# Kernel optimization log

Hardware: AMD Instinct MI355X
Metric: run time of the kernel (lower is better)

## Reference

```python
import jax, jax.numpy as jnp
import numpy as np

N = 100000   # nodes
F = 128      # feature dim (== numEdges ctor arg)
H = 64       # hidden_dim
E = 1600000  # edges (avg degree 16)


def setup_inputs() -> dict:
    key = jax.random.key(0)
    ks = jax.random.split(key, 8)
    x = jax.random.normal(ks[0], (N, F), dtype=jnp.float32)
    edge_index = jax.random.randint(ks[1], (2, E), 0, N)
    sF = 1.0 / np.sqrt(F)
    sH = 1.0 / np.sqrt(H)
    conv_W = jax.random.normal(ks[2], (F, F), dtype=jnp.float32) * sF  # GCNConv linear weight
    conv_b = jnp.zeros((F,), dtype=jnp.float32)
    w1 = jax.random.normal(ks[3], (H, F), dtype=jnp.float32) * sF
    b1 = jnp.zeros((H,), dtype=jnp.float32)
    w2 = jax.random.normal(ks[4], (H, H), dtype=jnp.float32) * sH
    b2 = jnp.zeros((H,), dtype=jnp.float32)
    w3 = jax.random.normal(ks[5], (1, H), dtype=jnp.float32) * sH
    b3 = jnp.zeros((1,), dtype=jnp.float32)
    return dict(x=x, edge_index=edge_index, conv_W=conv_W, conv_b=conv_b,
                w1=w1, b1=b1, w2=w2, b2=b2, w3=w3, b3=b3)


def reference(x, edge_index, conv_W, conv_b, w1, b1, w2, b2, w3, b3):
    n = x.shape[0]
    # --- GCNConv: D^{-1/2}(A+I)D^{-1/2} X W + b ---
    xw = x @ conv_W.T                                   # [N, F]
    loops = jnp.arange(n)
    src = jnp.concatenate([edge_index[0], loops])       # add self-loops
    dst = jnp.concatenate([edge_index[1], loops])
    deg = jax.ops.segment_sum(jnp.ones(src.shape[0], xw.dtype), dst, num_segments=n)
    dinv = jnp.where(deg > 0, jax.lax.rsqrt(deg), 0.0)
    norm = dinv[src] * dinv[dst]                        # [E+N]
    h = jax.ops.segment_sum(xw[src] * norm[:, None], dst, num_segments=n) + conv_b  # [N, F]
    # --- MedianAggregation (index=None -> single segment, 'lower' interpolation) ---
    med = jnp.sort(h, axis=0)[(n - 1) // 2][None, :]    # [1, F]
    # --- tanh MLP ---
    a = jnp.tanh(med @ w1.T + b1)
    a = jnp.tanh(a @ w2.T + b2)
    return a @ w3.T + b3                                # [1, 1]
```

## Files before the change

### kernel.cpp

```cpp
#include <hip/hip_runtime.h>
#include <math.h>


#define CAP    24576
#define NREG   8
#define RCAP   3072
#define MPT    24
#define CCAP   96
#define CSTR   97
#define DSTR   32
#define OVCAP  4096
#define SPCAP  2048
#define BCAP   4608
#define NBKMAX 400
#define CH     4096

typedef __attribute__((ext_vector_type(8))) short short8;
typedef __attribute__((ext_vector_type(4))) float f32x4;
typedef __attribute__((ext_vector_type(8))) _Float16 half8;
typedef __attribute__((ext_vector_type(2))) _Float16 half2v;

__device__ __forceinline__ unsigned ordKey(float x) {
    unsigned u = __float_as_uint(x);
    return (u & 0x80000000u) ? ~u : (u | 0x80000000u);
}
__device__ __forceinline__ unsigned short f2bf(float f) {
    unsigned u = __float_as_uint(f);
    return (unsigned short)((u + 0x7FFFu + ((u >> 16) & 1u)) >> 16);
}

__global__ void k_init(int* __restrict__ cursor, int* __restrict__ below8,
                       int* __restrict__ candCnt8, int* __restrict__ ovCnt,
                       const float* __restrict__ W, short* __restrict__ Whi,
                       short* __restrict__ Wlo, int nbk) {
    if (blockIdx.x == 1) {
        for (int idx = threadIdx.x; idx < 16384; idx += 256) {
            int j = idx & 7, lane = (idx >> 3) & 63;
            int t = (idx >> 9) & 7, s = idx >> 12;
            int row = t * 16 + (lane & 15);
            int k = s * 32 + (lane >> 4) * 8 + j;
            float w = W[row * 128 + k];
            unsigned short hb = f2bf(w);
            float hf = __uint_as_float((unsigned)hb << 16);
            Whi[idx] = (short)hb;
            Wlo[idx] = (short)f2bf(w - hf);
        }
        return;
    }
    int t = threadIdx.x;
    for (int i = t; i < nbk; i += 256) cursor[i] = 0;
    for (int i = t; i < NREG * 128; i += 256) { below8[i] = 0; candCnt8[i] = 0; }
    if (t == 0) { ovCnt[0] = 0; ovCnt[1] = 0; ovCnt[2] = 0; }
}

__global__ __launch_bounds__(256) void k_binGemm(
        const float* __restrict__ x, const short* __restrict__ Whi,
        const short* __restrict__ Wlo, _Float16* __restrict__ xw, int n, int GB,
        const int* __restrict__ src, const int* __restrict__ dst, int E,
        int* __restrict__ cursor, int2* __restrict__ binned,
        int* __restrict__ ovCnt, int2* __restrict__ ovBuf, int nbk) {
    __shared__ char smem[40960];
    const int t = threadIdx.x;
    if ((int)blockIdx.x < GB) {
        float* trn = (float*)smem;
        const int lane = t & 63, wv = t >> 6;
        const int quad = lane >> 4, m = lane & 15;
        const int rowBase = blockIdx.x * 64 + wv * 16;
        const int r = rowBase + m;
        const int rl = r < n ? r : (n - 1);
        f32x4 acc[8];
        #pragma unroll
        for (int q = 0; q < 8; q++) acc[q] = (f32x4){0.f, 0.f, 0.f, 0.f};
        #pragma unroll
        for (int s = 0; s < 4; s++) {
            const float* xp = x + (size_t)rl * 128 + s * 32 + quad * 8;
            float4 p0 = *(const float4*)xp;
            float4 p1 = *(const float4*)(xp + 4);
            float f[8] = {p0.x, p0.y, p0.z, p0.w, p1.x, p1.y, p1.z, p1.w};
            short8 ah, al;
            #pragma unroll
            for (int j = 0; j < 8; j++) {
                unsigned short hb = f2bf(f[j]);
                float hf = __uint_as_float((unsigned)hb << 16);
                ah[j] = (short)hb;
                al[j] = (short)f2bf(f[j] - hf);
            }
            #pragma unroll
            for (int q = 0; q < 8; q++) {
                short8 bh = *(const short8*)(Whi + (((s * 8 + q) * 64 + lane) << 3));
                short8 bl = *(const short8*)(Wlo + (((s * 8 + q) * 64 + lane) << 3));
                acc[q] = __builtin_amdgcn_mfma_f32_16x16x32_bf16(ah, bh, acc[q], 0, 0, 0);
                acc[q] = __builtin_amdgcn_mfma_f32_16x16x32_bf16(al, bh, acc[q], 0, 0, 0);
                acc[q] = __builtin_amdgcn_mfma_f32_16x16x32_bf16(ah, bl, acc[q], 0, 0, 0);
            }
        }
        float* tw = trn + wv * (16 * 132);
        #pragma unroll
        for (int q = 0; q < 8; q++)
            #pragma unroll
            for (int e = 0; e < 4; e++)
                tw[(quad * 4 + e) * 132 + q * 16 + m] = acc[q][e];
        #pragma unroll
        for (int i = 0; i < 4; i++) {
            int row = i * 4 + (lane >> 4);
            int c8 = lane & 15;
            const float* tp = tw + row * 132 + c8 * 8;
            float4 p0 = *(const float4*)tp;
            float4 p1 = *(const float4*)(tp + 4);
            half8 o;
            o[0] = (_Float16)p0.x; o[1] = (_Float16)p0.y;
            o[2] = (_Float16)p0.z; o[3] = (_Float16)p0.w;
            o[4] = (_Float16)p1.x; o[5] = (_Float16)p1.y;
            o[6] = (_Float16)p1.z; o[7] = (_Float16)p1.w;
            int grow = rowBase + row;
            if (grow < n) *(half8*)(xw + (size_t)grow * 128 + c8 * 8) = o;
        }
    } else {
        int2* sorted = (int2*)smem;
        int* hist  = (int*)(smem + 32768);
        int* gbase = hist + NBKMAX;
        int* lpre  = gbase + NBKMAX;
        int* hist2 = lpre + NBKMAX;
        int* sbase = hist2 + NBKMAX;
        int* wscan = sbase + NBKMAX;
        const int e0 = ((int)blockIdx.x - GB) * CH;
        const int len = min(CH, E - e0);
        for (int i = t; i < nbk; i += 256) { hist[i] = 0; hist2[i] = 0; }
        __syncthreads();
        for (int k = t; k < len; k += 256)
            atomicAdd(&hist[dst[e0 + k] >> 8], 1);
        __syncthreads();
        for (int i = t; i < nbk; i += 256) {
            int c = hist[i];
            if (c) {
                int g = atomicAdd(&cursor[i], c);
                if (g + c <= BCAP) gbase[i] = g;
                else {
                    gbase[i] = -1;
                    sbase[i] = atomicAdd(ovCnt, c);
                }
            }
        }
        {
            const int i0 = t * 2, i1 = i0 + 1;
            int h0 = (i0 < nbk) ? hist[i0] : 0;
            int h1 = (i1 < nbk) ? hist[i1] : 0;
            int s = h0 + h1;
            const int lane = t & 63, wv = t >> 6;
            int sc = s;
            #pragma unroll
            for (int off = 1; off < 64; off <<= 1) {
                int y = __shfl_up(sc, off, 64);
                if (lane >= off) sc += y;
            }
            if (lane == 63) wscan[wv] = sc;
            __syncthreads();
            int wbase = 0;
            for (int ww = 0; ww < wv; ww++) wbase += wscan[ww];
            int excl = wbase + sc - s;
            if (i0 < nbk) lpre[i0] = excl;
            if (i1 < nbk) lpre[i1] = excl + h0;
        }
        __syncthreads();
        for (int k = t; k < len; k += 256) {
            int s = src[e0 + k], d = dst[e0 + k];
            int b = d >> 8;
            int p = atomicAdd(&hist2[b], 1);
            sorted[lpre[b] + p] = make_int2(s, d);
        }
        __syncthreads();
        for (int k = t; k < len; k += 256) {
            int2 e = sorted[k];
            int b = e.y >> 8;
            int li = k - lpre[b];
            int g = gbase[b];
            if (g >= 0) binned[(size_t)b * BCAP + g + li] = e;
            else {
                int o = sbase[b] + li;
                if (o < OVCAP) ovBuf[o] = make_int2(e.y, e.x);
            }
        }
    }
}

__global__ __launch_bounds__(1024) void k_build(int2* __restrict__ binned,
                                                const int* __restrict__ cursor,
                                                float* __restrict__ dinv,
                                                unsigned char* __restrict__ deg8,
                                                int* __restrict__ ovCnt,
                                                int2* __restrict__ ovBuf,
                                                int* __restrict__ spillNodes, int n) {
    __shared__ int ladj[256 * DSTR];
    __shared__ int lcnt[256];
    const int b = blockIdx.x, t = threadIdx.x;
    const int cnt = min(cursor[b], BCAP);
    const size_t e0 = (size_t)b * BCAP;
    if (t < 256) lcnt[t] = 0;
    __syncthreads();
    for (int k = t; k < cnt; k += 1024) {
        int2 e = binned[e0 + k];
        int li = e.y & 255;
        int pos = atomicAdd(&lcnt[li], 1);
        if (pos < DSTR) ladj[li * DSTR + pos] = e.x;
        else {
            int o = atomicAdd(ovCnt, 1);
            if (o < OVCAP) ovBuf[o] = make_int2(e.y, e.x);
        }
    }
    __syncthreads();
    int4* adjOut = (int4*)((int*)binned + e0 * 2);
    const int4* lsrc4 = (const int4*)ladj;
    for (int i = t; i < 2048; i += 1024) adjOut[i] = lsrc4[i];
    if (t < 256) {
        int node = b * 256 + t;
        if (node < n) {
            int deg = lcnt[t];
            dinv[node] = (float)(1.0 / sqrt((double)(deg + 1)));
            deg8[node] = (unsigned char)(deg < 255 ? deg : 255);
            if (deg > DSTR) {
                int p = atomicAdd(ovCnt + 1, 1);
                if (p < SPCAP) spillNodes[p] = node;
            }
        }
    }
}

__global__ __launch_bounds__(256) void k_aggH(const _Float16* __restrict__ xw,
                                              const unsigned char* __restrict__ deg8,
                                              const int* __restrict__ adjAll,
                                              const float* __restrict__ dinv,
                                              const float* __restrict__ conv_b,
                                              _Float16* __restrict__ h, int n) {
    const int d = blockIdx.x * 4 + (threadIdx.x >> 6);
    if (d >= n) return;
    const int lane = threadIdx.x & 63;
    const int l32 = lane & 31;
    int degT = deg8[d];
    const int degB = degT < DSTR ? degT : DSTR;
    const float dd = dinv[d];
    const int* adjRow = adjAll + (size_t)(d >> 8) * (BCAP * 2) + (d & 255) * DSTR;
    int aj = adjRow[l32];
    bool ev = (lane < 32) && (l32 < degB);
    int ajs = ev ? aj : 0;
    float dv = ev ? dinv[ajs] : 0.f;
    const half2v* xwv = (const half2v*)xw;
    half2v a = xwv[(size_t)d * 64 + lane];
    float ax = dd * dd * (float)a.x, ay = dd * dd * (float)a.y;
    int j = 0;
    for (; j + 8 <= degB; j += 8) {
        int s[8];
        float w[8];
        #pragma unroll
        for (int q = 0; q < 8; q++) {
            s[q] = __shfl(ajs, j + q, 64);
            w[q] = dd * __shfl(dv, j + q, 64);
        }
        #pragma unroll
        for (int q = 0; q < 8; q++) {
            half2v v = xwv[(size_t)s[q] * 64 + lane];
            ax += w[q] * (float)v.x;
            ay += w[q] * (float)v.y;
        }
    }
    if (j < degB) {
        int s[8];
        float w[8];
        #pragma unroll
        for (int q = 0; q < 8; q++) {
            int idx = j + q;
            bool ok = idx < degB;
            int lsrc = ok ? idx : 0;
            int sv = __shfl(ajs, lsrc, 64);
            float wv = dd * __shfl(dv, lsrc, 64);
            s[q] = ok ? sv : 0;
            w[q] = ok ? wv : 0.f;
        }
        #pragma unroll
        for (int q = 0; q < 8; q++) {
            half2v v = xwv[(size_t)s[q] * 64 + lane];
            ax += w[q] * (float)v.x;
            ay += w[q] * (float)v.y;
        }
    }
    float2 cb = ((const float2*)conv_b)[lane];
    half2v o;
    o.x = (_Float16)(ax + cb.x);
    o.y = (_Float16)(ay + cb.y);
    ((half2v*)h)[(size_t)d * 64 + lane] = o;
}

__global__ __launch_bounds__(1024) void k_sampleSpill(
        _Float16* h, int n,
        unsigned* __restrict__ Lkey, unsigned* __restrict__ Ukey,
        const _Float16* __restrict__ xw, const int* __restrict__ spillNodes,
        const int* __restrict__ adjAll, const float* __restrict__ dinv,
        const float* __restrict__ conv_b, const int2* __restrict__ ovBuf,
        const int* __restrict__ ovCnt) {
    const int t = threadIdx.x;
    if (blockIdx.x >= 128) {
        int m = ovCnt[0];  if (m > OVCAP) m = OVCAP;
        int sp = ovCnt[1]; if (sp > SPCAP) sp = SPCAP;
        if (t >= 128) return;
        for (int i = (int)blockIdx.x - 128; i < sp; i += 16) {
            const int d = spillNodes[i];
            const float dd = dinv[d];
            float acc = dd * dd * (float)xw[(size_t)d * 128 + t];
            const int* adjRow = adjAll + (size_t)(d >> 8) * (BCAP * 2) + (d & 255) * DSTR;
            for (int j = 0; j < DSTR; j++) {
                int a = adjRow[j];
                acc += dd * dinv[a] * (float)xw[(size_t)a * 128 + t];
            }
            for (int k = 0; k < m; k++) {
                int2 e = ovBuf[k];
                if (e.x == d)
                    acc += dd * dinv[e.y] * (float)xw[(size_t)e.y * 128 + t];
            }
            h[(size_t)d * 128 + t] = (_Float16)(acc + conv_b[t]);
        }
        return;
    }
    __shared__ int hist[2048];
    __shared__ int wsum[4];
    const int c = blockIdx.x;
    for (int i = t; i < 2048; i += 1024) hist[i] = 0;
    __syncthreads();
    const int ns = (n + 31) >> 5;
    for (int i = t; i < ns; i += 1024) {
        float v = (float)h[(size_t)(i << 5) * 128 + c];
        atomicAdd(&hist[ordKey(v) >> 21], 1);
    }
    __syncthreads();
    int ps = 0, sc = 0;
    const int lane = t & 63, wv = t >> 6;
    if (t < 256) {
        #pragma unroll
        for (int b = 0; b < 8; b++) ps += hist[t * 8 + b];
        sc = ps;
        #pragma unroll
        for (int off = 1; off < 64; off <<= 1) {
            int y = __shfl_up(sc, off, 64);
            if (lane >= off) sc += y;
        }
        if (lane == 63) wsum[wv] = sc;
    }
    __syncthreads();
    if (t < 256) {
        int wbase = 0;
        for (int ww = 0; ww < wv; ww++) wbase += wsum[ww];
        const int excl = wbase + sc - ps;
        const int sMid = (ns - 1) >> 1;
        const int delta = (int)(4.0f * sqrtf((float)ns)) + 1;
        int sLo = sMid - delta; if (sLo < 0) sLo = 0;
        int sHi = sMid + delta; if (sHi > ns - 1) sHi = ns - 1;
        if (sLo >= excl && sLo < excl + ps) {
            int rem = sLo - excl, b = t * 8;
            for (;; b++) { int cc = hist[b]; if (rem < cc) break; rem -= cc; }
            Lkey[c] = (unsigned)b << 21;
        }
        if (sHi >= excl && sHi < excl + ps) {
            int rem = sHi - excl, b = t * 8;
            for (;; b++) { int cc = hist[b]; if (rem < cc) break; rem -= cc; }
            Ukey[c] = (((unsigned)(b + 1)) << 21) - 1u;
        }
    }
}

__global__ __launch_bounds__(256) void k_classify(const _Float16* __restrict__ h,
                                                  int total8,
                                                  const unsigned* __restrict__ Lkey,
                                                  const unsigned* __restrict__ Ukey,
                                                  int* __restrict__ below8,
                                                  int* __restrict__ candCnt8,
                                                  _Float16* __restrict__ cand) {
    __shared__ _Float16 buf[128 * CSTR];
    __shared__ int cN[128], cB[128];
    const int t = threadIdx.x;
    const int rid = (int)blockIdx.x & (NREG - 1);
    for (int i = t; i < 128; i += 256) { cN[i] = 0; cB[i] = 0; }
    __syncthreads();
    const int stride = gridDim.x * blockDim.x;
    const int i0 = blockIdx.x * blockDim.x + t;
    const int jb = (i0 << 3) & 127;
    unsigned L[8], U[8];
    #pragma unroll
    for (int k = 0; k < 8; k++) { L[k] = Lkey[jb + k]; U[k] = Ukey[jb + k]; }
    int b[8] = {0, 0, 0, 0, 0, 0, 0, 0};
    const half8* hv = (const half8*)h;
    for (int i = i0; i < total8; i += stride) {
        half8 v = hv[i];
        #pragma unroll
        for (int k = 0; k < 8; k++) {
            float f = (float)v[k];
            unsigned u = ordKey(f);
            if (u < L[k]) b[k]++;
            else if (u <= U[k]) {
                int p = atomicAdd(&cN[jb + k], 1);
                if (p < CCAP) buf[(jb + k) * CSTR + p] = v[k];
                else {
                    int g = atomicAdd(&candCnt8[rid * 128 + jb + k], 1);
                    if (g < RCAP)
                        cand[(size_t)(jb + k) * CAP + rid * RCAP + g] = v[k];
                }
            }
        }
    }
    #pragma unroll
    for (int k = 0; k < 8; k++)
        if (b[k]) atomicAdd(&cB[jb + k], b[k]);
    __syncthreads();
    if (t < 128) {
        if (cB[t]) atomicAdd(&below8[rid * 128 + t], cB[t]);
        int nn = cN[t] < CCAP ? cN[t] : CCAP;
        if (nn) {
            int base = atomicAdd(&candCnt8[rid * 128 + t], nn);
            for (int k2 = 0; k2 < nn && base + k2 < RCAP; k2++)
                cand[(size_t)t * CAP + rid * RCAP + base + k2] = buf[t * CSTR + k2];
        }
    }
}

__global__ __launch_bounds__(1024) void k_finalMlp(
        const _Float16* __restrict__ cand, const int* __restrict__ candCnt8,
        const int* __restrict__ below8, int n, float* __restrict__ med,
        int* __restrict__ doneCnt,
        const float* __restrict__ w1, const float* __restrict__ b1,
        const float* __restrict__ w2, const float* __restrict__ b2,
        const float* __restrict__ w3, const float* __restrict__ b3,
        float* __restrict__ out) {
    __shared__ int wsum[16];
    __shared__ int lastFlag;
    const int c = blockIdx.x, t = threadIdx.x;
    const int lane = t & 63, wv = t >> 6;
    int below_tot = 0;
    #pragma unroll
    for (int rr = 0; rr < NREG; rr++) below_tot += below8[rr * 128 + c];
    int cnt = 0;
    unsigned short myk[MPT];
    const unsigned short* cbase = (const unsigned short*)cand + (size_t)c * CAP;
    #pragma unroll
    for (int rr = 0; rr < NREG; rr++) {
        int cr = candCnt8[rr * 128 + c]; if (cr > RCAP) cr = RCAP;
        cnt += cr;
        const unsigned short* rp = cbase + rr * RCAP;
        #pragma unroll
        for (int k = 0; k < RCAP / 1024; k++) {
            int i = t + k * 1024;
            unsigned ub = (i < cr) ? (unsigned)rp[i] : 0u;
            unsigned kk = (ub & 0x8000u) ? (~ub & 0xFFFFu) : (ub | 0x8000u);
            myk[rr * (RCAP / 1024) + k] =
                (i < cr) ? (unsigned short)kk : (unsigned short)0xFFFFu;
        }
    }
    int r = (n - 1) / 2 - below_tot;
    if (r < 0) r = 0;
    if (r >= cnt) r = cnt - 1;
    unsigned cur = 0;
    for (int bit = 15; bit >= 0; bit--) {
        const unsigned pivot = cur | (1u << bit);
        int lc = 0;
        #pragma unroll
        for (int mi = 0; mi < MPT; mi++) lc += ((unsigned)myk[mi] < pivot) ? 1 : 0;
        #pragma unroll
        for (int off = 32; off > 0; off >>= 1) lc += __shfl_down(lc, off, 64);
        if (lane == 0) wsum[wv] = lc;
        __syncthreads();
        int tot = 0;
        #pragma unroll
        for (int ww = 0; ww < 16; ww++) tot += wsum[ww];
        if (tot <= r) cur = pivot;
        __syncthreads();
    }
    if (t == 0) {
        unsigned short bits = (cur & 0x8000u) ? (unsigned short)(cur & 0x7FFFu)
                                              : (unsigned short)(~cur & 0xFFFFu);
        _Float16 hv;
        *(unsigned short*)&hv = bits;
        med[c] = (float)hv;
        __threadfence();
        int old = atomicAdd(doneCnt, 1);
        lastFlag = (old == 127);
    }
    __syncthreads();
    if (!lastFlag) return;
    __threadfence();
    __shared__ float m[128], a1[64], a2[64];
    if (t < 128) m[t] = med[t];
    __syncthreads();
    if (t < 64) {
        float acc = b1[t];
        for (int f = 0; f < 128; f++) acc += m[f] * w1[t * 128 + f];
        a1[t] = tanhf(acc);
    }
    __syncthreads();
    if (t < 64) {
        float acc = b2[t];
        for (int f = 0; f < 64; f++) acc += a1[f] * w2[t * 64 + f];
        a2[t] = tanhf(acc);
    }
    __syncthreads();
    if (t == 0) {
        float acc = b3[0];
        for (int f = 0; f < 64; f++) acc += a2[f] * w3[f];
        out[0] = acc;
    }
}

extern "C" void kernel_launch(void* const* d_in, const int* in_sizes, int n_in,
                              void* d_out, int out_size, void* d_ws, size_t ws_size,
                              hipStream_t stream) {
    const float* x      = (const float*)d_in[0];
    const int*   ei     = (const int*)d_in[1];
    const float* conv_W = (const float*)d_in[2];
    const float* conv_b = (const float*)d_in[3];
    const float* w1 = (const float*)d_in[4];
    const float* b1 = (const float*)d_in[5];
    const float* w2 = (const float*)d_in[6];
    const float* b2 = (const float*)d_in[7];
    const float* w3 = (const float*)d_in[8];
    const float* b3 = (const float*)d_in[9];

    const int N = in_sizes[0] / 128;
    const int E = in_sizes[1] / 2;
    const int* src = ei;
    const int* dst = ei + E;
    const int NBK = (N + 255) / 256;

    char* p = (char*)d_ws;
    auto alloc = [&](size_t bytes) -> char* {
        char* q = p;
        p += (bytes + 255) & ~(size_t)255;
        return q;
    };
    _Float16* xw  = (_Float16*)alloc((size_t)N * 128 * 2);
    _Float16* h   = (_Float16*)alloc((size_t)N * 128 * 2);
    int2*  binned = (int2*)alloc((size_t)NBK * BCAP * 8);
    _Float16* cand = (_Float16*)alloc((size_t)128 * CAP * 2);
    float* dinv   = (float*)alloc((size_t)N * 4);
    unsigned char* deg8 = (unsigned char*)alloc((size_t)N);
    int*   cursor = (int*)alloc((size_t)NBK * 4);
    short* Whi    = (short*)alloc(16384 * 2);
    short* Wlo    = (short*)alloc(16384 * 2);
    int2*  ovBuf  = (int2*)alloc((size_t)OVCAP * 8);
    int*   ovCnt  = (int*)alloc(256);
    int*   spillNodes = (int*)alloc((size_t)SPCAP * 4);
    unsigned* Lkey = (unsigned*)alloc(128 * 4);
    unsigned* Ukey = (unsigned*)alloc(128 * 4);
    int*   below8   = (int*)alloc((size_t)NREG * 128 * 4);
    int*   candCnt8 = (int*)alloc((size_t)NREG * 128 * 4);
    float* med     = (float*)alloc(128 * 4);

    const int GB   = (N + 63) / 64;
    const int BINB = (E + CH - 1) / CH;

    k_init<<<2, 256, 0, stream>>>(cursor, below8, candCnt8, ovCnt, conv_W,
                                  Whi, Wlo, NBK);
    k_binGemm<<<GB + BINB, 256, 0, stream>>>(x, Whi, Wlo, xw, N, GB,
                                             src, dst, E, cursor, binned,
                                             ovCnt, ovBuf, NBK);
    k_build<<<NBK, 1024, 0, stream>>>(binned, cursor, dinv, deg8, ovCnt, ovBuf,
                                      spillNodes, N);
    k_aggH<<<(N + 3) / 4, 256, 0, stream>>>(xw, deg8, (const int*)binned, dinv,
                                            conv_b, h, N);
    k_sampleSpill<<<144, 1024, 0, stream>>>(h, N, Lkey, Ukey, xw, spillNodes,
                                            (const int*)binned, dinv, conv_b,
                                            ovBuf, ovCnt);
    k_classify<<<512, 256, 0, stream>>>(h, N * 16, Lkey, Ukey, below8, candCnt8,
                                        cand);
    k_finalMlp<<<128, 1024, 0, stream>>>(cand, candCnt8, below8, N, med,
                                         ovCnt + 2, w1, b1, w2, b2, w3, b3,
                                         (float*)d_out);
}
```

Before: 279.1 us.

## Split aggregation per half-wave node and feature half across blocks

The gather-aggregation kernel now gives each half-wave one destination node and one half of the feature columns (64 of 128). Consecutive block groups handle the two feature halves for the same 32 nodes. Each 32-lane group uses the lanes that previously idled during index loading, and each gathered row segment is 128 bytes instead of 256. In exchange, adjacency and dinv are loaded twice per node, and the two nodes sharing a wave iterate to the larger of their degrees with masked loads. The tail handling is also merged into the main loop.

```diff
diff --git a/kernel.cpp b/kernel.cpp
--- a/kernel.cpp
+++ b/kernel.cpp
@@ -231,62 +231,51 @@
                                               const float* __restrict__ dinv,
                                               const float* __restrict__ conv_b,
                                               _Float16* __restrict__ h, int n) {
-    const int d = blockIdx.x * 4 + (threadIdx.x >> 6);
-    if (d >= n) return;
-    const int lane = threadIdx.x & 63;
-    const int l32 = lane & 31;
-    int degT = deg8[d];
-    const int degB = degT < DSTR ? degT : DSTR;
-    const float dd = dinv[d];
-    const int* adjRow = adjAll + (size_t)(d >> 8) * (BCAP * 2) + (d & 255) * DSTR;
+    const int b = blockIdx.x;
+    const int hf = (b >> 2) & 1;
+    const int g = (b >> 3) * 4 + (b & 3);
+    const int t = threadIdx.x;
+    const int lane = t & 63, wv = t >> 6;
+    const int sub = lane >> 5, l32 = lane & 31;
+    const int d = g * 8 + wv * 2 + sub;
+    const int dl = d < n ? d : (n - 1);
+    int myDeg = deg8[dl]; if (myDeg > DSTR) myDeg = DSTR;
+    const float dd = dinv[dl];
+    const int* adjRow = adjAll + (size_t)(dl >> 8) * (BCAP * 2) + (dl & 255) * DSTR;
     int aj = adjRow[l32];
-    bool ev = (lane < 32) && (l32 < degB);
+    bool ev = l32 < myDeg;
     int ajs = ev ? aj : 0;
     float dv = ev ? dinv[ajs] : 0.f;
+    int degW = max(myDeg, __shfl_xor(myDeg, 32, 64));
     const half2v* xwv = (const half2v*)xw;
-    half2v a = xwv[(size_t)d * 64 + lane];
+    const int co = hf * 32 + l32;
+    half2v a = xwv[(size_t)dl * 64 + co];
     float ax = dd * dd * (float)a.x, ay = dd * dd * (float)a.y;
-    int j = 0;
-    for (; j + 8 <= degB; j += 8) {
+    for (int j = 0; j < degW; j += 8) {
         int s[8];
         float w[8];
         #pragma unroll
         for (int q = 0; q < 8; q++) {
-            s[q] = __shfl(ajs, j + q, 64);
-            w[q] = dd * __shfl(dv, j + q, 64);
+            bool ok = (j + q) < myDeg;
+            int sv = __shfl(ajs, j + q, 32);
+            float wv2 = dd * __shfl(dv, j + q, 32);
+            s[q] = ok ? sv : 0;
+            w[q] = ok ? wv2 : 0.f;
         }
         #pragma unroll
         for (int q = 0; q < 8; q++) {
-            half2v v = xwv[(size_t)s[q] * 64 + lane];
+            half2v v = xwv[(size_t)s[q] * 64 + co];
             ax += w[q] * (float)v.x;
             ay += w[q] * (float)v.y;
         }
     }
-    if (j < degB) {
-        int s[8];
-        float w[8];
-        #pragma unroll
-        for (int q = 0; q < 8; q++) {
-            int idx = j + q;
-            bool ok = idx < degB;
-            int lsrc = ok ? idx : 0;
-            int sv = __shfl(ajs, lsrc, 64);
-            float wv = dd * __shfl(dv, lsrc, 64);
-            s[q] = ok ? sv : 0;
-            w[q] = ok ? wv : 0.f;
-        }
-        #pragma unroll
-        for (int q = 0; q < 8; q++) {
-            half2v v = xwv[(size_t)s[q] * 64 + lane];
-            ax += w[q] * (float)v.x;
-            ay += w[q] * (float)v.y;
-        }
-    }
-    float2 cb = ((const float2*)conv_b)[lane];
-    half2v o;
-    o.x = (_Float16)(ax + cb.x);
-    o.y = (_Float16)(ay + cb.y);
-    ((half2v*)h)[(size_t)d * 64 + lane] = o;
+    if (d < n) {
+        float2 cb = ((const float2*)conv_b)[co];
+        half2v o;
+        o.x = (_Float16)(ax + cb.x);
+        o.y = (_Float16)(ay + cb.y);
+        ((half2v*)h)[(size_t)d * 64 + co] = o;
+    }
 }
 
 __global__ __launch_bounds__(1024) void k_sampleSpill(
@@ -551,6 +540,7 @@
 
     const int GB   = (N + 63) / 64;
     const int BINB = (E + CH - 1) / CH;
+    const int NG4  = (((N + 7) / 8) + 3) / 4;
 
     k_init<<<2, 256, 0, stream>>>(cursor, below8, candCnt8, ovCnt, conv_W,
                                   Whi, Wlo, NBK);
@@ -559,8 +549,8 @@
                                              ovCnt, ovBuf, NBK);
     k_build<<<NBK, 1024, 0, stream>>>(binned, cursor, dinv, deg8, ovCnt, ovBuf,
                                       spillNodes, N);
-    k_aggH<<<(N + 3) / 4, 256, 0, stream>>>(xw, deg8, (const int*)binned, dinv,
-                                            conv_b, h, N);
+    k_aggH<<<NG4 * 8, 256, 0, stream>>>(xw, deg8, (const int*)binned, dinv,
+                                        conv_b, h, N);
     k_sampleSpill<<<144, 1024, 0, stream>>>(h, N, Lkey, Ukey, xw, spillNodes,
                                             (const int*)binned, dinv, conv_b,
                                             ovBuf, ovCnt);
```

New measurement: 276.6 us. No clear change (-0.9%).
